# Kernel optimization log

Hardware: AMD Instinct MI355X
Metric: run time of the kernel (lower is better)

## Reference

```python
import jax, jax.numpy as jnp
import numpy as np

B, L, d, D = 256, 128, 2, 128  # batch, sites, local dim, bond dim


def setup_inputs() -> dict:
    key = jax.random.key(0)
    k1, k2 = jax.random.split(key)
    # local quantum-number indices (output of hilbert.states_to_local_indices)
    x = jax.random.randint(k1, (B, L), 0, d, dtype=jnp.int32)
    # MPS unit-cell tensors: kernel_init (normal, std=0.01) + identity, as in setup()
    tensors = 0.01 * jax.random.normal(k2, (L, d, D, D), dtype=jnp.float32) \
        + jnp.eye(D, dtype=jnp.float32)
    return {"x": x, "tensors": tensors}


def reference(x, tensors):
    # x: (B, L) int indices in [0, d); tensors: (L, d, D, D)
    # symperiod == L so the tile in __call__ is a no-op.
    Bn, Ln = x.shape
    Dn = tensors.shape[-1]
    edge0 = jnp.broadcast_to(jnp.eye(Dn, dtype=tensors.dtype), (Bn, Dn, Dn))

    @jax.checkpoint
    def step(edge, pair):
        site_tensors, qn = pair          # (d, D, D), (B,)
        a = site_tensors[qn]             # gather per-sample matrix -> (B, D, D)
        return edge @ a, None            # batched (B,D,D)@(B,D,D)

    edge, _ = jax.lax.scan(step, edge0, (tensors, x.T))
    psi = jnp.trace(edge, axis1=-2, axis2=-1)     # (B,)
    return jnp.log(psi.astype(jnp.complex64))
```

## Files before the change

### kernel.cpp

```cpp
#include <hip/hip_runtime.h>
#include <cstdint>

#define DD   128
#define LL   128
#define MAT  (DD*DD)
#define ROWB 256

typedef float  f32x16 __attribute__((ext_vector_type(16)));
typedef short  bf16x8 __attribute__((ext_vector_type(8)));
typedef unsigned short u16_t;

__device__ u16_t g_A  [LL*2*MAT];
__device__ u16_t g_At [LL*2*MAT];
__device__ u16_t g_M2 [64*4*MAT];
__device__ u16_t g_M2t[64*4*MAT];
__device__ u16_t g_M4t[32*16*MAT];

__device__ __forceinline__ u16_t f2bf(float f){
  unsigned int x = __builtin_bit_cast(unsigned int, f);
  unsigned int r = (x + 0x7FFFu + ((x >> 16) & 1u)) >> 16;
  return (u16_t)r;
}
__device__ __forceinline__ float bf2f(u16_t u){
  unsigned int x = ((unsigned int)u) << 16;
  return __builtin_bit_cast(float, x);
}
__device__ __forceinline__ f32x16 mfma32(bf16x8 a, bf16x8 b, f32x16 c){
  return __builtin_amdgcn_mfma_f32_32x32x16_bf16(a, b, c, 0, 0, 0);
}
__device__ __forceinline__ f32x16 zero16(){
  f32x16 z;
#pragma unroll
  for (int i = 0; i < 16; ++i) z[i] = 0.f;
  return z;
}
__device__ __forceinline__ unsigned cvtpk(float lo, float hi){
  unsigned r;
  asm("v_cvt_pk_bf16_f32 %0, %1, %2" : "=v"(r) : "v"(lo), "v"(hi));
  return r;
}
__device__ __forceinline__ void pl32swap(unsigned &a, unsigned &b){
  asm volatile("v_permlane32_swap_b32 %0, %1" : "+v"(a), "+v"(b));
}

__device__ __forceinline__ bf16x8 ldfrag(const u16_t* base, int row, int ko){
  int xr = (row & 15) << 4;
  return *(const bf16x8*)((const char*)base + row*ROWB + (ko ^ xr));
}

__device__ __forceinline__ void stage32k(u16_t* dstLds, const u16_t* srcG, int tid){
  int w = tid >> 6, l = tid & 63;
  const char* g = (const char*)srcG + w*8192 + l*16;
  char* s = (char*)dstLds + w*8192;
#pragma unroll
  for (int i = 0; i < 8; ++i){
    __builtin_amdgcn_global_load_lds(
      (const __attribute__((address_space(1))) unsigned int*)(uintptr_t)(g + i*1024),
      (__attribute__((address_space(3))) unsigned int*)(unsigned int)(uintptr_t)(s + i*1024),
      16, 0, 0);
  }
}

__global__ __launch_bounds__(256, 1) void k_convert(const float* __restrict__ T){
  __shared__ float tile[128][129];
  const int lq = blockIdx.x, tid = threadIdx.x;
  const float* src = T + (size_t)lq * MAT;
#pragma unroll 4
  for (int i = 0; i < 64; ++i){
    int idx = tid + 256*i;
    float v = src[idx];
    g_A[lq*MAT + idx] = f2bf(v);
    tile[idx >> 7][idx & 127] = v;
  }
  __syncthreads();
#pragma unroll 4
  for (int i = 0; i < 64; ++i){
    int idx = tid + 256*i;
    int c = idx >> 7, k = idx & 127;
    g_At[lq*MAT + idx] = f2bf(tile[k][c]);
  }
}

__global__ __launch_bounds__(256, 1) void k_prod(int level){
  __shared__ u16_t CT[MAT];
  __shared__ u16_t CR[MAT];
  const int bid = blockIdx.x, tid = threadIdx.x;
  const int w = tid >> 6, lane = tid & 63, g = lane >> 5, ln = lane & 31;
  const int wr = (w >> 1) * 64, wc = (w & 1) * 64;

  const u16_t *X, *Yt; u16_t *Z, *Zt; bool sw;
  if (level == 1){
    int p = bid >> 2, c2 = bid & 3;
    X  = g_A  + ((2*p)*2   + (c2 & 1)) * MAT;
    Yt = g_At + ((2*p+1)*2 + ((c2 >> 1) & 1)) * MAT;
    Z  = g_M2  + bid*MAT;
    Zt = g_M2t + bid*MAT;
    sw = false;
  } else {
    int gg = bid >> 4, c = bid & 15;
    X  = g_M2  + ((2*gg)*4   + (c & 3)) * MAT;
    Yt = g_M2t + ((2*gg+1)*4 + (c >> 2)) * MAT;
    Z  = nullptr;
    Zt = g_M4t + bid*MAT;
    sw = true;
  }

  f32x16 acc[2][2];
  acc[0][0] = zero16(); acc[0][1] = zero16();
  acc[1][0] = zero16(); acc[1][1] = zero16();

#pragma unroll
  for (int kw = 0; kw < 8; ++kw){
    int ko = kw*32 + g*16;
    bf16x8 a0 = *(const bf16x8*)((const char*)X  + (wr + ln     )*ROWB + ko);
    bf16x8 a1 = *(const bf16x8*)((const char*)X  + (wr + 32 + ln)*ROWB + ko);
    bf16x8 b0 = *(const bf16x8*)((const char*)Yt + (wc + ln     )*ROWB + ko);
    bf16x8 b1 = *(const bf16x8*)((const char*)Yt + (wc + 32 + ln)*ROWB + ko);
    acc[0][0] = mfma32(a0, b0, acc[0][0]);
    acc[0][1] = mfma32(a0, b1, acc[0][1]);
    acc[1][0] = mfma32(a1, b0, acc[1][0]);
    acc[1][1] = mfma32(a1, b1, acc[1][1]);
  }

#pragma unroll
  for (int mt = 0; mt < 2; ++mt){
#pragma unroll
    for (int nt = 0; nt < 2; ++nt){
      int c  = wc + nt*32 + ln;
      int xc = (c & 15) << 4;
#pragma unroll
      for (int q = 0; q < 4; ++q){
        int r4 = wr + mt*32 + 8*q + 4*g;
        unsigned int lo = (unsigned)f2bf(acc[mt][nt][4*q+0]) | ((unsigned)f2bf(acc[mt][nt][4*q+1]) << 16);
        unsigned int hi = (unsigned)f2bf(acc[mt][nt][4*q+2]) | ((unsigned)f2bf(acc[mt][nt][4*q+3]) << 16);
        uint2 v; v.x = lo; v.y = hi;
        *(uint2*)((char*)CT + c*ROWB + ((2*r4) ^ xc)) = v;
      }
      if (level == 1){
#pragma unroll
        for (int i = 0; i < 16; ++i){
          int r = wr + mt*32 + (i & 3) + 8*(i >> 2) + 4*g;
          *(u16_t*)((char*)CR + r*ROWB + ((2*c) ^ ((r & 15) << 4))) = f2bf(acc[mt][nt][i]);
        }
      }
    }
  }
  __syncthreads();

#pragma unroll
  for (int i = 0; i < 8; ++i){
    int o = (tid + 256*i) * 16;
    int row = o >> 8, wb = o & 255;
    int xr = (row & 15) << 4;
    uint4 vt = *(const uint4*)((const char*)CT + row*ROWB + (sw ? wb : (wb ^ xr)));
    *(uint4*)((char*)Zt + o) = vt;
    if (level == 1){
      uint4 vz = *(const uint4*)((const char*)CR + row*ROWB + (wb ^ xr));
      *(uint4*)((char*)Z + o) = vz;
    }
  }
}

#define LDS_MAIN (2*32768 + 128 + 128)

__global__ __launch_bounds__(256, 1) void k_main(const int* __restrict__ x,
                                                 float* __restrict__ out,
                                                 int out_complex){
  extern __shared__ char lds[];
  u16_t* M0 = (u16_t*)lds;
  u16_t* M1 = M0 + MAT;
  int*   combo = (int*)(M1 + MAT);
  float* red   = (float*)(combo + 32);

  const int b = blockIdx.x, tid = threadIdx.x;
  const int w = tid >> 6, lane = tid & 63, g = lane >> 5, ln = lane & 31;

  if (tid < 32){
    const int* xb = x + b*LL + tid*4;
    combo[tid] = (xb[0] & 1) | ((xb[1] & 1) << 1) | ((xb[2] & 1) << 2) | ((xb[3] & 1) << 3);
  }
  __syncthreads();
  stage32k(M0, g_M4t + (size_t)(0*16 + combo[0])*MAT, tid);

  uint4 F[8];
#pragma unroll
  for (int kw = 0; kw < 8; ++kw){
    unsigned wd[4] = {0u,0u,0u,0u};
#pragma unroll
    for (int j = 0; j < 8; ++j){
      int k = 16*kw + 8*g + j;
      if (k == 32*w + ln) wd[j >> 1] |= 0x3F80u << (16*(j & 1));
    }
    uint4 v; v.x = wd[0]; v.y = wd[1]; v.z = wd[2]; v.w = wd[3];
    F[kw] = v;
  }
  __syncthreads();

  for (int t = 0; t < 32; ++t){
    const u16_t* Mc = (t & 1) ? M1 : M0;
    u16_t*       Mn = (t & 1) ? M0 : M1;
    if (t + 1 < 32) stage32k(Mn, g_M4t + (size_t)((t+1)*16 + combo[t+1])*MAT, tid);

    f32x16 acc[4];
#pragma unroll
    for (int rt = 0; rt < 4; ++rt) acc[rt] = zero16();

#pragma unroll
    for (int kw = 0; kw < 8; ++kw){
      bf16x8 bb = __builtin_bit_cast(bf16x8, F[kw]);
#pragma unroll
      for (int rt = 0; rt < 4; ++rt){
        bf16x8 a = ldfrag(Mc, 32*rt + ln, kw*32 + g*16);
        acc[rt] = mfma32(a, bb, acc[rt]);
      }
    }

#pragma unroll
    for (int rt = 0; rt < 4; ++rt){
      unsigned y0 = cvtpk(acc[rt][0],  acc[rt][1]);
      unsigned x0 = cvtpk(acc[rt][4],  acc[rt][5]);
      pl32swap(y0, x0);
      unsigned y1 = cvtpk(acc[rt][2],  acc[rt][3]);
      unsigned x1 = cvtpk(acc[rt][6],  acc[rt][7]);
      pl32swap(y1, x1);
      uint4 v0; v0.x = y0; v0.y = y1; v0.z = x0; v0.w = x1;
      F[2*rt] = v0;

      unsigned y2 = cvtpk(acc[rt][8],  acc[rt][9]);
      unsigned x2 = cvtpk(acc[rt][12], acc[rt][13]);
      pl32swap(y2, x2);
      unsigned y3 = cvtpk(acc[rt][10], acc[rt][11]);
      unsigned x3 = cvtpk(acc[rt][14], acc[rt][15]);
      pl32swap(y3, x3);
      uint4 v1; v1.x = y2; v1.y = y3; v1.z = x2; v1.w = x3;
      F[2*rt+1] = v1;
    }
    __syncthreads();
  }

  int cg = 32*w + ln;
  float dval = 0.f;
  if (((cg >> 3) & 1) == g){
    int kwn = (cg >> 4), jn = cg & 7;
#pragma unroll
    for (int kw = 0; kw < 8; ++kw) if (kw == kwn){
      uint4 v = F[kw];
#pragma unroll
      for (int j = 0; j < 8; ++j) if (j == jn){
        unsigned word = (j >> 1) == 0 ? v.x : ((j >> 1) == 1 ? v.y : ((j >> 1) == 2 ? v.z : v.w));
        u16_t bits = (u16_t)((j & 1) ? (word >> 16) : (word & 0xFFFF));
        dval = bf2f(bits);
      }
    }
  }
#pragma unroll
  for (int off = 1; off < 64; off <<= 1) dval += __shfl_xor(dval, off, 64);
  if (lane == 0) red[w] = dval;
  __syncthreads();
  if (tid == 0){
    float s = red[0] + red[1] + red[2] + red[3];
    float re = logf(fabsf(s));
    float im = (s < 0.f) ? 3.14159265358979323f : 0.f;
    if (out_complex){ out[2*b] = re; out[2*b+1] = im; }
    else            { out[b] = re; }
  }
}

extern "C" void kernel_launch(void* const* d_in, const int* in_sizes, int n_in,
                              void* d_out, int out_size, void* d_ws, size_t ws_size,
                              hipStream_t stream){
  const int*   x = (const int*)d_in[0];
  const float* T = (const float*)d_in[1];
  int Bn = in_sizes[0] / LL;
  int oc = (out_size >= 2*Bn) ? 1 : 0;

  (void)d_ws; (void)ws_size; (void)n_in;
  hipFuncSetAttribute(reinterpret_cast<const void*>(k_main),
                      hipFuncAttributeMaxDynamicSharedMemorySize, LDS_MAIN);

  k_convert<<<LL*2, 256, 0, stream>>>(T);
  k_prod   <<<256,  256, 0, stream>>>(1);
  k_prod   <<<512,  256, 0, stream>>>(2);
  k_main   <<<Bn,   256, LDS_MAIN, stream>>>(x, (float*)d_out, oc);
}
```

Before: 87.43 us.

## Split each sample's chain into two halves and combine them via trace kernel

The main kernel now launches two blocks per sample, each multiplying 16 of the 32 precomputed 4-site matrices, which doubles the parallelism over the sequential chain. The level-2 product kernel writes its output in MFMA fragment order, so the main loop loads fragments straight from global memory and drops the LDS staging and double buffering. A new tail kernel computes trace(F0·F1) as an elementwise dot product over the two half-products, written to global scratch buffers. This adds an extra launch, global round-trips of 256 pairs of 32KB matrices, and scattered 2-byte transposed stores in the second half.

```diff
diff --git a/kernel.cpp b/kernel.cpp
--- a/kernel.cpp
+++ b/kernel.cpp
@@ -15,6 +15,8 @@
 __device__ u16_t g_M2 [64*4*MAT];
 __device__ u16_t g_M2t[64*4*MAT];
 __device__ u16_t g_M4t[32*16*MAT];
+__device__ u16_t g_F0 [256*MAT];
+__device__ u16_t g_F1 [256*MAT];
 
 __device__ __forceinline__ u16_t f2bf(float f){
   unsigned int x = __builtin_bit_cast(unsigned int, f);
@@ -41,24 +43,6 @@
 }
 __device__ __forceinline__ void pl32swap(unsigned &a, unsigned &b){
   asm volatile("v_permlane32_swap_b32 %0, %1" : "+v"(a), "+v"(b));
-}
-
-__device__ __forceinline__ bf16x8 ldfrag(const u16_t* base, int row, int ko){
-  int xr = (row & 15) << 4;
-  return *(const bf16x8*)((const char*)base + row*ROWB + (ko ^ xr));
-}
-
-__device__ __forceinline__ void stage32k(u16_t* dstLds, const u16_t* srcG, int tid){
-  int w = tid >> 6, l = tid & 63;
-  const char* g = (const char*)srcG + w*8192 + l*16;
-  char* s = (char*)dstLds + w*8192;
-#pragma unroll
-  for (int i = 0; i < 8; ++i){
-    __builtin_amdgcn_global_load_lds(
-      (const __attribute__((address_space(1))) unsigned int*)(uintptr_t)(g + i*1024),
-      (__attribute__((address_space(3))) unsigned int*)(unsigned int)(uintptr_t)(s + i*1024),
-      16, 0, 0);
-  }
 }
 
 __global__ __launch_bounds__(256, 1) void k_convert(const float* __restrict__ T){
@@ -88,21 +72,19 @@
   const int w = tid >> 6, lane = tid & 63, g = lane >> 5, ln = lane & 31;
   const int wr = (w >> 1) * 64, wc = (w & 1) * 64;
 
-  const u16_t *X, *Yt; u16_t *Z, *Zt; bool sw;
+  const u16_t *X, *Yt; u16_t *Z, *Zt;
   if (level == 1){
     int p = bid >> 2, c2 = bid & 3;
     X  = g_A  + ((2*p)*2   + (c2 & 1)) * MAT;
     Yt = g_At + ((2*p+1)*2 + ((c2 >> 1) & 1)) * MAT;
     Z  = g_M2  + bid*MAT;
     Zt = g_M2t + bid*MAT;
-    sw = false;
   } else {
     int gg = bid >> 4, c = bid & 15;
     X  = g_M2  + ((2*gg)*4   + (c & 3)) * MAT;
     Yt = g_M2t + ((2*gg+1)*4 + (c >> 2)) * MAT;
     Z  = nullptr;
     Zt = g_M4t + bid*MAT;
-    sw = true;
   }
 
   f32x16 acc[2][2];
@@ -147,40 +129,42 @@
   }
   __syncthreads();
 
-#pragma unroll
-  for (int i = 0; i < 8; ++i){
-    int o = (tid + 256*i) * 16;
-    int row = o >> 8, wb = o & 255;
-    int xr = (row & 15) << 4;
-    uint4 vt = *(const uint4*)((const char*)CT + row*ROWB + (sw ? wb : (wb ^ xr)));
-    *(uint4*)((char*)Zt + o) = vt;
-    if (level == 1){
+  if (level == 1){
+#pragma unroll
+    for (int i = 0; i < 8; ++i){
+      int o = (tid + 256*i) * 16;
+      int row = o >> 8, wb = o & 255;
+      int xr = (row & 15) << 4;
+      uint4 vt = *(const uint4*)((const char*)CT + row*ROWB + (wb ^ xr));
+      *(uint4*)((char*)Zt + o) = vt;
       uint4 vz = *(const uint4*)((const char*)CR + row*ROWB + (wb ^ xr));
       *(uint4*)((char*)Z + o) = vz;
     }
-  }
-}
-
-#define LDS_MAIN (2*32768 + 128 + 128)
-
-__global__ __launch_bounds__(256, 1) void k_main(const int* __restrict__ x,
-                                                 float* __restrict__ out,
-                                                 int out_complex){
-  extern __shared__ char lds[];
-  u16_t* M0 = (u16_t*)lds;
-  u16_t* M1 = M0 + MAT;
-  int*   combo = (int*)(M1 + MAT);
-  float* red   = (float*)(combo + 32);
-
-  const int b = blockIdx.x, tid = threadIdx.x;
+  } else {
+#pragma unroll
+    for (int i = 0; i < 8; ++i){
+      int o = tid + 256*i;
+      int lnn = o & 31, ggg = (o >> 5) & 1, kww = (o >> 6) & 7, rtt = o >> 9;
+      int r = 32*rtt + lnn;
+      int srcB = r*ROWB + ((32*kww + 16*ggg) ^ ((r & 15) << 4));
+      uint4 v = *(const uint4*)((const char*)CT + srcB);
+      *(uint4*)((char*)Zt + o*16) = v;
+    }
+  }
+}
+
+__global__ __launch_bounds__(256, 1) void k_main(const int* __restrict__ x){
+  __shared__ int combo[16];
+
+  const int bid = blockIdx.x;
+  const int b = bid & 255, half = bid >> 8;
+  const int tid = threadIdx.x;
   const int w = tid >> 6, lane = tid & 63, g = lane >> 5, ln = lane & 31;
 
-  if (tid < 32){
-    const int* xb = x + b*LL + tid*4;
+  if (tid < 16){
+    const int* xb = x + b*LL + (half*16 + tid)*4;
     combo[tid] = (xb[0] & 1) | ((xb[1] & 1) << 1) | ((xb[2] & 1) << 2) | ((xb[3] & 1) << 3);
   }
-  __syncthreads();
-  stage32k(M0, g_M4t + (size_t)(0*16 + combo[0])*MAT, tid);
 
   uint4 F[8];
 #pragma unroll
@@ -196,10 +180,9 @@
   }
   __syncthreads();
 
-  for (int t = 0; t < 32; ++t){
-    const u16_t* Mc = (t & 1) ? M1 : M0;
-    u16_t*       Mn = (t & 1) ? M0 : M1;
-    if (t + 1 < 32) stage32k(Mn, g_M4t + (size_t)((t+1)*16 + combo[t+1])*MAT, tid);
+  for (int t = 0; t < 16; ++t){
+    const u16_t* Mg = g_M4t + (size_t)(((half*16 + t)*16) + combo[t]) * MAT;
+    const char*  Ml = (const char*)Mg + lane*16;
 
     f32x16 acc[4];
 #pragma unroll
@@ -210,7 +193,7 @@
       bf16x8 bb = __builtin_bit_cast(bf16x8, F[kw]);
 #pragma unroll
       for (int rt = 0; rt < 4; ++rt){
-        bf16x8 a = ldfrag(Mc, 32*rt + ln, kw*32 + g*16);
+        bf16x8 a = *(const bf16x8*)(Ml + (rt*8 + kw)*1024);
         acc[rt] = mfma32(a, bb, acc[rt]);
       }
     }
@@ -235,27 +218,57 @@
       uint4 v1; v1.x = y2; v1.y = y3; v1.z = x2; v1.w = x3;
       F[2*rt+1] = v1;
     }
-    __syncthreads();
-  }
-
-  int cg = 32*w + ln;
-  float dval = 0.f;
-  if (((cg >> 3) & 1) == g){
-    int kwn = (cg >> 4), jn = cg & 7;
-#pragma unroll
-    for (int kw = 0; kw < 8; ++kw) if (kw == kwn){
+    __builtin_amdgcn_s_barrier();
+  }
+
+  const int c = 32*w + ln;
+  if (half == 0){
+    u16_t* dst = g_F0 + (size_t)b*MAT + c*128;
+#pragma unroll
+    for (int kw = 0; kw < 8; ++kw)
+      *(uint4*)(dst + kw*16 + g*8) = F[kw];
+  } else {
+    u16_t* dst = g_F1 + (size_t)b*MAT + c;
+#pragma unroll
+    for (int kw = 0; kw < 8; ++kw){
       uint4 v = F[kw];
-#pragma unroll
-      for (int j = 0; j < 8; ++j) if (j == jn){
-        unsigned word = (j >> 1) == 0 ? v.x : ((j >> 1) == 1 ? v.y : ((j >> 1) == 2 ? v.z : v.w));
-        u16_t bits = (u16_t)((j & 1) ? (word >> 16) : (word & 0xFFFF));
-        dval = bf2f(bits);
-      }
-    }
-  }
-#pragma unroll
-  for (int off = 1; off < 64; off <<= 1) dval += __shfl_xor(dval, off, 64);
-  if (lane == 0) red[w] = dval;
+      unsigned wd[4] = {v.x, v.y, v.z, v.w};
+#pragma unroll
+      for (int j = 0; j < 8; ++j){
+        int k = 16*kw + 8*g + j;
+        u16_t bits = (u16_t)((j & 1) ? (wd[j >> 1] >> 16) : (wd[j >> 1] & 0xFFFF));
+        dst[(size_t)k*128] = bits;
+      }
+    }
+  }
+}
+
+__global__ __launch_bounds__(256, 1) void k_tail(float* __restrict__ out,
+                                                 int out_complex){
+  __shared__ float red[4];
+  const int b = blockIdx.x, tid = threadIdx.x;
+  const int w = tid >> 6, lane = tid & 63;
+
+  const u16_t* S0 = g_F0 + (size_t)b*MAT;
+  const u16_t* W  = g_F1 + (size_t)b*MAT;
+
+  float sum = 0.f;
+#pragma unroll
+  for (int i = 0; i < 8; ++i){
+    int o = (i*256 + tid)*8;
+    uint4 a = *(const uint4*)(S0 + o);
+    uint4 v = *(const uint4*)(W  + o);
+    unsigned aw[4] = {a.x, a.y, a.z, a.w};
+    unsigned vw[4] = {v.x, v.y, v.z, v.w};
+#pragma unroll
+    for (int q = 0; q < 4; ++q){
+      sum += bf2f((u16_t)(aw[q] & 0xFFFF)) * bf2f((u16_t)(vw[q] & 0xFFFF));
+      sum += bf2f((u16_t)(aw[q] >> 16))    * bf2f((u16_t)(vw[q] >> 16));
+    }
+  }
+#pragma unroll
+  for (int off = 1; off < 64; off <<= 1) sum += __shfl_xor(sum, off, 64);
+  if (lane == 0) red[w] = sum;
   __syncthreads();
   if (tid == 0){
     float s = red[0] + red[1] + red[2] + red[3];
@@ -275,11 +288,10 @@
   int oc = (out_size >= 2*Bn) ? 1 : 0;
 
   (void)d_ws; (void)ws_size; (void)n_in;
-  hipFuncSetAttribute(reinterpret_cast<const void*>(k_main),
-                      hipFuncAttributeMaxDynamicSharedMemorySize, LDS_MAIN);
-
-  k_convert<<<LL*2, 256, 0, stream>>>(T);
-  k_prod   <<<256,  256, 0, stream>>>(1);
-  k_prod   <<<512,  256, 0, stream>>>(2);
-  k_main   <<<Bn,   256, LDS_MAIN, stream>>>(x, (float*)d_out, oc);
-}
+
+  k_convert<<<LL*2,  256, 0, stream>>>(T);
+  k_prod   <<<256,   256, 0, stream>>>(1);
+  k_prod   <<<512,   256, 0, stream>>>(2);
+  k_main   <<<2*Bn,  256, 0, stream>>>(x);
+  k_tail   <<<Bn,    256, 0, stream>>>((float*)d_out, oc);
+}
```

Result: slower. 173.5 us (+98.4%).
